# Performance work log

Measured on AMD Instinct MI355X. Metric: run time of the kernel, lower is better.

## Reference

```python
import jax, jax.numpy as jnp
import numpy as np

TEMP = 0.2
EPS = 1e-12  # F.normalize eps


def setup_inputs() -> dict:
    key = jax.random.key(0)
    k1, k2 = jax.random.split(key)
    l, B, K, D = 4, 64, 32, 128
    emb_i = jax.random.normal(k1, (l, B, K, D), dtype=jnp.float32)
    emb_j = jax.random.normal(k2, (l, B, K, D), dtype=jnp.float32)
    joint_valid = jnp.ones((B, K), dtype=jnp.float32)
    return {"emb_i": emb_i, "emb_j": emb_j, "joint_valid": joint_valid}


def _l2norm(x):
    n = jnp.sqrt(jnp.sum(x * x, axis=-1, keepdims=True))
    return x / jnp.maximum(n, EPS)


def reference(emb_i, emb_j, joint_valid):
    l, B, K, D = emb_i.shape
    N = B * K
    z_i = _l2norm(emb_i.reshape(l, N, D))
    z_j = _l2norm(emb_j.reshape(l, N, D))
    reps = jnp.concatenate([z_i, z_j], axis=1)              # (l, 2N, D), unit rows
    # cosine similarity of unit vectors == matmul
    sim = jnp.einsum('lnd,lmd->lnm', reps, reps)            # (l, 2N, 2N)
    idx = jnp.arange(N)
    pos = sim[:, idx, idx + N]                              # diag offset +N, (l, N)
    # note: original code uses the SAME +N offset diagonal for both ij and ji
    positives = jnp.concatenate([pos, pos], axis=1)         # (l, 2N)
    neg_mask = 1.0 - jnp.eye(2 * N, dtype=sim.dtype)        # (2N, 2N)
    denom = jnp.sum(neg_mask[None] * jnp.exp(sim / TEMP), axis=2)  # (l, 2N)
    loss_partial = -jnp.log(jnp.exp(positives / TEMP) / denom)    # (l, 2N)
    joints_mask = joint_valid.reshape(1, 1, B, K)
    all_num = jnp.sum(joint_valid)
    loss = jnp.sum(loss_partial.reshape(l, 2, B, K) * joints_mask) / (2.0 * all_num)
    return loss
```

## Files before the change

### kernel.cpp

```cpp
#include <hip/hip_runtime.h>
#include <hip/hip_bf16.h>

typedef __attribute__((ext_vector_type(8))) short short8;
typedef __attribute__((ext_vector_type(4))) float floatx4;

#define NROWS 4096
#define NHALF 2048
#define DDIM  128
#define LDST  136
#define SQRT_SCALE 2.6857914f
#define LN2 0.69314718056f

#define WS_ROWSUM_OFF 64
#define WS_DIAG_OFF   16448
#define WS_POS_OFF    32832
#define WS_Z_BYTE_OFF 196864

__device__ inline unsigned short f2bf(float f) {
    unsigned u = __builtin_bit_cast(unsigned, f);
    u += 0x7fffu + ((u >> 16) & 1u);
    return (unsigned short)(u >> 16);
}

__global__ __launch_bounds__(256) void k_norm(const float* __restrict__ emb_i,
                                              const float* __restrict__ emb_j,
                                              const float* __restrict__ jv,
                                              float* __restrict__ wsf,
                                              unsigned short* __restrict__ z) {
    int bx = blockIdx.x, tid = threadIdx.x;
    if (bx == 4096) {
        __shared__ float sred[256];
        float s = 0.f;
        #pragma unroll
        for (int i = 0; i < 8; ++i) s += jv[tid + 256 * i];
        sred[tid] = s; __syncthreads();
        for (int off = 128; off > 0; off >>= 1) {
            if (tid < off) sred[tid] += sred[tid + off];
            __syncthreads();
        }
        if (tid == 0) wsf[1] = sred[0];
        return;
    }
    int gid = bx * 256 + tid;
    if (gid == 0) { wsf[0] = 0.f; *(unsigned*)&wsf[2] = 0u; }
    if (gid >= WS_ROWSUM_OFF && gid < WS_ROWSUM_OFF + 16384) wsf[gid] = 0.f;

    int wave = tid >> 6, lane = tid & 63;
    int r = bx * 4 + wave;
    int l = r >> 12, n = r & 4095;
    const float* src = (n < NHALF) ? (emb_i + ((size_t)l * NHALF + n) * DDIM)
                                   : (emb_j + ((size_t)l * NHALF + (n - NHALF)) * DDIM);
    float2 v = *(const float2*)(src + lane * 2);
    float ss = v.x * v.x + v.y * v.y;
    #pragma unroll
    for (int off = 1; off < 64; off <<= 1) ss += __shfl_xor(ss, off);
    float inv = SQRT_SCALE / fmaxf(sqrtf(ss), 1e-12f);
    unsigned pack = ((unsigned)f2bf(v.y * inv) << 16) | (unsigned)f2bf(v.x * inv);
    *(unsigned*)(z + (size_t)r * DDIM + lane * 2) = pack;
}

__global__ __launch_bounds__(256, 4) void k_sim(const unsigned short* __restrict__ z,
                                                float* __restrict__ rowsum,
                                                float* __restrict__ diag,
                                                float* __restrict__ pos) {
    __shared__ __align__(16) unsigned short lds[128 * LDST];
    int bx = blockIdx.x, tid = threadIdx.x;
    int l = bx & 3, idx = bx >> 2;
    int J = (int)((sqrtf(8.f * (float)idx + 1.f) - 1.f) * 0.5f);
    while ((J + 1) * (J + 2) / 2 <= idx) ++J;
    while (J * (J + 1) / 2 > idx) --J;
    int I = idx - J * (J + 1) / 2;
    int wave = tid >> 6, lane = tid & 63, m = lane & 15, quad = lane >> 4;
    const unsigned short* zl = z + (size_t)l * NROWS * DDIM;
    int l4 = l * NROWS;
    int wr0 = I * 128 + wave * 32;
    int cg0 = J * 128;

    short8 a[2][4];
    #pragma unroll
    for (int rs = 0; rs < 2; ++rs) {
        const unsigned short* p = zl + (size_t)(wr0 + rs * 16 + m) * DDIM + quad * 8;
        #pragma unroll
        for (int kk = 0; kk < 4; ++kk) a[rs][kk] = *(const short8*)(p + kk * 32);
    }
    floatx4 rsum[2];
    #pragma unroll
    for (int rs = 0; rs < 2; ++rs) rsum[rs] = (floatx4){0.f, 0.f, 0.f, 0.f};
    float csum[8];
    #pragma unroll
    for (int g = 0; g < 8; ++g) csum[g] = 0.f;

    #pragma unroll
    for (int i = 0; i < 8; ++i) {
        int chunk = tid + 256 * i;
        int col = chunk >> 4, off = chunk & 15;
        uint4 d = *(const uint4*)(zl + (size_t)(cg0 + col) * DDIM + off * 8);
        *(uint4*)&lds[col * LDST + off * 8] = d;
    }
    __syncthreads();

    #pragma unroll
    for (int cs = 0; cs < 8; ++cs) {
        int ct = cg0 + cs * 16;
        const unsigned short* lp = &lds[(cs * 16 + m) * LDST + quad * 8];
        short8 b0 = *(const short8*)(lp);
        short8 b1 = *(const short8*)(lp + 32);
        short8 b2 = *(const short8*)(lp + 64);
        short8 b3 = *(const short8*)(lp + 96);
        #pragma unroll
        for (int rs = 0; rs < 2; ++rs) {
            floatx4 acc = (floatx4){0.f, 0.f, 0.f, 0.f};
            acc = __builtin_amdgcn_mfma_f32_16x16x32_bf16(a[rs][0], b0, acc, 0, 0, 0);
            acc = __builtin_amdgcn_mfma_f32_16x16x32_bf16(a[rs][1], b1, acc, 0, 0, 0);
            acc = __builtin_amdgcn_mfma_f32_16x16x32_bf16(a[rs][2], b2, acc, 0, 0, 0);
            acc = __builtin_amdgcn_mfma_f32_16x16x32_bf16(a[rs][3], b3, acc, 0, 0, 0);
            int rowbase = wr0 + rs * 16;
            bool isdiag = (ct == rowbase);
            bool ispos  = (ct == rowbase + 2048);
            if (isdiag || ispos) {
                int c = m - (quad << 2);
                if (c >= 0 && c < 4) {
                    float v = acc[c];
                    if (isdiag) diag[l4 + rowbase + m] = v;
                    else {
                        pos[l4 + rowbase + m] = v;
                        pos[l4 + rowbase + m + NHALF] = v;
                    }
                }
            }
            float t = 0.f;
            #pragma unroll
            for (int c = 0; c < 4; ++c) {
                float e = __builtin_amdgcn_exp2f(acc[c]);
                rsum[rs][c] += e;
                t += e;
            }
            csum[cs] += t;
        }
    }
    #pragma unroll
    for (int off = 1; off < 16; off <<= 1)
        #pragma unroll
        for (int rs = 0; rs < 2; ++rs)
            #pragma unroll
            for (int c = 0; c < 4; ++c)
                rsum[rs][c] += __shfl_xor(rsum[rs][c], off);
    if (m == 0) {
        #pragma unroll
        for (int rs = 0; rs < 2; ++rs)
            #pragma unroll
            for (int c = 0; c < 4; ++c) {
                int rg = wr0 + rs * 16 + quad * 4 + c;
                atomicAdd(&rowsum[l4 + rg], rsum[rs][c]);
            }
    }
    if (I != J) {
        __syncthreads();
        float* cred = (float*)lds;
        #pragma unroll
        for (int g = 0; g < 8; ++g) {
            float v = csum[g];
            v += __shfl_xor(v, 16);
            v += __shfl_xor(v, 32);
            if (quad == 0) cred[wave * 128 + g * 16 + m] = v;
        }
        __syncthreads();
        if (tid < 128) {
            float s = cred[tid] + cred[tid + 128] + cred[tid + 256] + cred[tid + 384];
            atomicAdd(&rowsum[l4 + cg0 + tid], s);
        }
    }
}

__global__ __launch_bounds__(256) void k_loss(const float* __restrict__ jv,
                                              const float* __restrict__ rowsum,
                                              const float* __restrict__ diag,
                                              const float* __restrict__ pos,
                                              float* __restrict__ wsf,
                                              float* __restrict__ out) {
    __shared__ float sred[256];
    int tid = threadIdx.x;
    int r = blockIdx.x * 256 + tid;
    int n = r & 4095;
    float denom = rowsum[r] - __builtin_amdgcn_exp2f(diag[r]);
    float contrib = LN2 * (__builtin_amdgcn_logf(denom) - pos[r]);
    float local = contrib * jv[n & (NHALF - 1)];
    sred[tid] = local; __syncthreads();
    for (int off = 128; off > 0; off >>= 1) {
        if (tid < off) sred[tid] += sred[tid + off];
        __syncthreads();
    }
    if (tid == 0) {
        atomicAdd(&wsf[0], sred[0]);
        __threadfence();
        unsigned c = atomicAdd((unsigned*)&wsf[2], 1u);
        if (c == 63) {
            float tot = atomicAdd(&wsf[0], 0.f);
            out[0] = tot / (2.f * wsf[1]);
        }
    }
}

extern "C" void kernel_launch(void* const* d_in, const int* in_sizes, int n_in,
                              void* d_out, int out_size, void* d_ws, size_t ws_size,
                              hipStream_t stream) {
    const float* emb_i = (const float*)d_in[0];
    const float* emb_j = (const float*)d_in[1];
    const float* jv    = (const float*)d_in[2];
    float* wsf    = (float*)d_ws;
    float* rowsum = wsf + WS_ROWSUM_OFF;
    float* diag   = wsf + WS_DIAG_OFF;
    float* pos    = wsf + WS_POS_OFF;
    unsigned short* z = (unsigned short*)((char*)d_ws + WS_Z_BYTE_OFF);
    float* out = (float*)d_out;

    k_norm <<<4097, 256, 0, stream>>>(emb_i, emb_j, jv, wsf, z);
    k_sim  <<<2112, 256, 0, stream>>>(z, rowsum, diag, pos);
    k_loss <<<64,   256, 0, stream>>>(jv, rowsum, diag, pos, wsf, out);
}
```

Measured before the change: 88.04 us.

## Pair row tiles per block and replace atomics with per-tile partial sums

Each k_sim block now handles two row tiles against one shared LDS column tile, which halves the grid and reuses each B-tile load across twice the MFMA work. Row and column exp-sums are written without atomics into a per-(layer, column tile) partial buffer. k_loss then sums 32 partials per row, so the zeroing pass in k_norm is removed. The costs are higher register pressure (launch bounds lowered to 3 blocks per CU), a larger workspace, and extra reads in k_loss.

After: 99.44 us. 12.9% more time.

```diff
diff --git a/kernel.cpp b/kernel.cpp
--- a/kernel.cpp
+++ b/kernel.cpp
@@ -11,10 +11,10 @@
 #define SQRT_SCALE 2.6857914f
 #define LN2 0.69314718056f
 
-#define WS_ROWSUM_OFF 64
-#define WS_DIAG_OFF   16448
-#define WS_POS_OFF    32832
-#define WS_Z_BYTE_OFF 196864
+#define WS_PART_OFF 64
+#define WS_DIAG_OFF 524352
+#define WS_POS_OFF  540736
+#define WS_Z_BYTE_OFF 2228480
 
 __device__ inline unsigned short f2bf(float f) {
     unsigned u = __builtin_bit_cast(unsigned, f);
@@ -41,9 +41,7 @@
         if (tid == 0) wsf[1] = sred[0];
         return;
     }
-    int gid = bx * 256 + tid;
-    if (gid == 0) { wsf[0] = 0.f; *(unsigned*)&wsf[2] = 0u; }
-    if (gid >= WS_ROWSUM_OFF && gid < WS_ROWSUM_OFF + 16384) wsf[gid] = 0.f;
+    if (bx == 0 && tid == 0) { wsf[0] = 0.f; *(unsigned*)&wsf[2] = 0u; }
 
     int wave = tid >> 6, lane = tid & 63;
     int r = bx * 4 + wave;
@@ -59,37 +57,38 @@
     *(unsigned*)(z + (size_t)r * DDIM + lane * 2) = pack;
 }
 
-__global__ __launch_bounds__(256, 4) void k_sim(const unsigned short* __restrict__ z,
-                                                float* __restrict__ rowsum,
+#define CPAIR(j) (((j) & 1) ? ((((j)+1)>>1)*(((j)+1)>>1)) : (((j)*((j)+2))>>2))
+__global__ __launch_bounds__(256, 3) void k_sim(const unsigned short* __restrict__ z,
+                                                float* __restrict__ part,
                                                 float* __restrict__ diag,
                                                 float* __restrict__ pos) {
     __shared__ __align__(16) unsigned short lds[128 * LDST];
+    __shared__ float cred[2][4][128];
     int bx = blockIdx.x, tid = threadIdx.x;
-    int l = bx & 3, idx = bx >> 2;
-    int J = (int)((sqrtf(8.f * (float)idx + 1.f) - 1.f) * 0.5f);
-    while ((J + 1) * (J + 2) / 2 <= idx) ++J;
-    while (J * (J + 1) / 2 > idx) --J;
-    int I = idx - J * (J + 1) / 2;
+    int l = bx & 3, q = bx >> 2;
+    int J = (int)(2.f * sqrtf((float)q + 0.25f));
+    if (J > 31) J = 31;
+    while (J < 31 && CPAIR(J + 1) <= q) ++J;
+    while (CPAIR(J) > q) --J;
+    int p = q - CPAIR(J);
+    int I0 = 2 * p;
+    bool two = (2 * p + 1 <= J);
+    int I1 = two ? (2 * p + 1) : I0;
+
     int wave = tid >> 6, lane = tid & 63, m = lane & 15, quad = lane >> 4;
     const unsigned short* zl = z + (size_t)l * NROWS * DDIM;
     int l4 = l * NROWS;
-    int wr0 = I * 128 + wave * 32;
     int cg0 = J * 128;
-
-    short8 a[2][4];
+    int wr00 = I0 * 128 + wave * 32;
+    int wr10 = I1 * 128 + wave * 32;
+
+    short8 a0[2][4], a1[2][4];
     #pragma unroll
     for (int rs = 0; rs < 2; ++rs) {
-        const unsigned short* p = zl + (size_t)(wr0 + rs * 16 + m) * DDIM + quad * 8;
-        #pragma unroll
-        for (int kk = 0; kk < 4; ++kk) a[rs][kk] = *(const short8*)(p + kk * 32);
-    }
-    floatx4 rsum[2];
-    #pragma unroll
-    for (int rs = 0; rs < 2; ++rs) rsum[rs] = (floatx4){0.f, 0.f, 0.f, 0.f};
-    float csum[8];
-    #pragma unroll
-    for (int g = 0; g < 8; ++g) csum[g] = 0.f;
-
+        const unsigned short* pa = zl + (size_t)(wr00 + rs * 16 + m) * DDIM + quad * 8;
+        #pragma unroll
+        for (int kk = 0; kk < 4; ++kk) a0[rs][kk] = *(const short8*)(pa + kk * 32);
+    }
     #pragma unroll
     for (int i = 0; i < 8; ++i) {
         int chunk = tid + 256 * i;
@@ -97,6 +96,21 @@
         uint4 d = *(const uint4*)(zl + (size_t)(cg0 + col) * DDIM + off * 8);
         *(uint4*)&lds[col * LDST + off * 8] = d;
     }
+    #pragma unroll
+    for (int rs = 0; rs < 2; ++rs) {
+        const unsigned short* pa = zl + (size_t)(wr10 + rs * 16 + m) * DDIM + quad * 8;
+        #pragma unroll
+        for (int kk = 0; kk < 4; ++kk) a1[rs][kk] = *(const short8*)(pa + kk * 32);
+    }
+    floatx4 rsum0[2], rsum1[2];
+    float csum0[8], csum1[8];
+    #pragma unroll
+    for (int rs = 0; rs < 2; ++rs) {
+        rsum0[rs] = (floatx4){0.f, 0.f, 0.f, 0.f};
+        rsum1[rs] = (floatx4){0.f, 0.f, 0.f, 0.f};
+    }
+    #pragma unroll
+    for (int g = 0; g < 8; ++g) { csum0[g] = 0.f; csum1[g] = 0.f; }
     __syncthreads();
 
     #pragma unroll
@@ -107,73 +121,91 @@
         short8 b1 = *(const short8*)(lp + 32);
         short8 b2 = *(const short8*)(lp + 64);
         short8 b3 = *(const short8*)(lp + 96);
+        float t0 = 0.f, t1 = 0.f;
         #pragma unroll
         for (int rs = 0; rs < 2; ++rs) {
-            floatx4 acc = (floatx4){0.f, 0.f, 0.f, 0.f};
-            acc = __builtin_amdgcn_mfma_f32_16x16x32_bf16(a[rs][0], b0, acc, 0, 0, 0);
-            acc = __builtin_amdgcn_mfma_f32_16x16x32_bf16(a[rs][1], b1, acc, 0, 0, 0);
-            acc = __builtin_amdgcn_mfma_f32_16x16x32_bf16(a[rs][2], b2, acc, 0, 0, 0);
-            acc = __builtin_amdgcn_mfma_f32_16x16x32_bf16(a[rs][3], b3, acc, 0, 0, 0);
-            int rowbase = wr0 + rs * 16;
-            bool isdiag = (ct == rowbase);
-            bool ispos  = (ct == rowbase + 2048);
-            if (isdiag || ispos) {
+            floatx4 p0 = (floatx4){0.f, 0.f, 0.f, 0.f};
+            floatx4 p1 = (floatx4){0.f, 0.f, 0.f, 0.f};
+            p0 = __builtin_amdgcn_mfma_f32_16x16x32_bf16(a0[rs][0], b0, p0, 0, 0, 0);
+            p1 = __builtin_amdgcn_mfma_f32_16x16x32_bf16(a1[rs][0], b0, p1, 0, 0, 0);
+            p0 = __builtin_amdgcn_mfma_f32_16x16x32_bf16(a0[rs][1], b1, p0, 0, 0, 0);
+            p1 = __builtin_amdgcn_mfma_f32_16x16x32_bf16(a1[rs][1], b1, p1, 0, 0, 0);
+            p0 = __builtin_amdgcn_mfma_f32_16x16x32_bf16(a0[rs][2], b2, p0, 0, 0, 0);
+            p1 = __builtin_amdgcn_mfma_f32_16x16x32_bf16(a1[rs][2], b2, p1, 0, 0, 0);
+            p0 = __builtin_amdgcn_mfma_f32_16x16x32_bf16(a0[rs][3], b3, p0, 0, 0, 0);
+            p1 = __builtin_amdgcn_mfma_f32_16x16x32_bf16(a1[rs][3], b3, p1, 0, 0, 0);
+            int rb0 = wr00 + rs * 16, rb1 = wr10 + rs * 16;
+            bool d0 = (ct == rb0), s0 = (ct == rb0 + 2048);
+            bool d1 = (ct == rb1), s1 = (ct == rb1 + 2048);
+            if (d0 || s0) {
                 int c = m - (quad << 2);
                 if (c >= 0 && c < 4) {
-                    float v = acc[c];
-                    if (isdiag) diag[l4 + rowbase + m] = v;
-                    else {
-                        pos[l4 + rowbase + m] = v;
-                        pos[l4 + rowbase + m + NHALF] = v;
-                    }
+                    float v = p0[c];
+                    if (d0) diag[l4 + rb0 + m] = v;
+                    else { pos[l4 + rb0 + m] = v; pos[l4 + rb0 + m + NHALF] = v; }
                 }
             }
-            float t = 0.f;
+            if (d1 || s1) {
+                int c = m - (quad << 2);
+                if (c >= 0 && c < 4) {
+                    float v = p1[c];
+                    if (d1) diag[l4 + rb1 + m] = v;
+                    else { pos[l4 + rb1 + m] = v; pos[l4 + rb1 + m + NHALF] = v; }
+                }
+            }
             #pragma unroll
             for (int c = 0; c < 4; ++c) {
-                float e = __builtin_amdgcn_exp2f(acc[c]);
-                rsum[rs][c] += e;
-                t += e;
-            }
-            csum[cs] += t;
-        }
+                float e0 = __builtin_amdgcn_exp2f(p0[c]);
+                float e1 = __builtin_amdgcn_exp2f(p1[c]);
+                rsum0[rs][c] += e0; t0 += e0;
+                rsum1[rs][c] += e1; t1 += e1;
+            }
+        }
+        csum0[cs] += t0;
+        csum1[cs] += t1;
     }
     #pragma unroll
     for (int off = 1; off < 16; off <<= 1)
-        #pragma unroll
-        for (int rs = 0; rs < 2; ++rs)
-            #pragma unroll
-            for (int c = 0; c < 4; ++c)
-                rsum[rs][c] += __shfl_xor(rsum[rs][c], off);
-    if (m == 0) {
         #pragma unroll
         for (int rs = 0; rs < 2; ++rs)
             #pragma unroll
             for (int c = 0; c < 4; ++c) {
-                int rg = wr0 + rs * 16 + quad * 4 + c;
-                atomicAdd(&rowsum[l4 + rg], rsum[rs][c]);
-            }
-    }
-    if (I != J) {
-        __syncthreads();
-        float* cred = (float*)lds;
-        #pragma unroll
-        for (int g = 0; g < 8; ++g) {
-            float v = csum[g];
-            v += __shfl_xor(v, 16);
-            v += __shfl_xor(v, 32);
-            if (quad == 0) cred[wave * 128 + g * 16 + m] = v;
-        }
-        __syncthreads();
-        if (tid < 128) {
-            float s = cred[tid] + cred[tid + 128] + cred[tid + 256] + cred[tid + 384];
-            atomicAdd(&rowsum[l4 + cg0 + tid], s);
+                rsum0[rs][c] += __shfl_xor(rsum0[rs][c], off);
+                rsum1[rs][c] += __shfl_xor(rsum1[rs][c], off);
+            }
+    float* plJ = part + (size_t)(l * 32 + J) * 4096;
+    if (m == 0) {
+        #pragma unroll
+        for (int rs = 0; rs < 2; ++rs)
+            #pragma unroll
+            for (int c = 0; c < 4; ++c) {
+                plJ[wr00 + rs * 16 + quad * 4 + c] = rsum0[rs][c];
+                if (two) plJ[wr10 + rs * 16 + quad * 4 + c] = rsum1[rs][c];
+            }
+    }
+    #pragma unroll
+    for (int g = 0; g < 8; ++g) {
+        float v0 = csum0[g]; v0 += __shfl_xor(v0, 16); v0 += __shfl_xor(v0, 32);
+        float v1 = csum1[g]; v1 += __shfl_xor(v1, 16); v1 += __shfl_xor(v1, 32);
+        if (quad == 0) { cred[0][wave][g * 16 + m] = v0; cred[1][wave][g * 16 + m] = v1; }
+    }
+    __syncthreads();
+    if (tid < 128) {
+        if (I0 != J) {
+            float s = cred[0][0][tid] + cred[0][1][tid] + cred[0][2][tid] + cred[0][3][tid];
+            part[(size_t)(l * 32 + I0) * 4096 + cg0 + tid] = s;
+        }
+    } else {
+        if (two && I1 != J) {
+            int t = tid - 128;
+            float s = cred[1][0][t] + cred[1][1][t] + cred[1][2][t] + cred[1][3][t];
+            part[(size_t)(l * 32 + I1) * 4096 + cg0 + t] = s;
         }
     }
 }
 
 __global__ __launch_bounds__(256) void k_loss(const float* __restrict__ jv,
-                                              const float* __restrict__ rowsum,
+                                              const float* __restrict__ part,
                                               const float* __restrict__ diag,
                                               const float* __restrict__ pos,
                                               float* __restrict__ wsf,
@@ -181,8 +213,12 @@
     __shared__ float sred[256];
     int tid = threadIdx.x;
     int r = blockIdx.x * 256 + tid;
-    int n = r & 4095;
-    float denom = rowsum[r] - __builtin_amdgcn_exp2f(diag[r]);
+    int l = r >> 12, n = r & 4095;
+    const float* pl = part + (size_t)l * 32 * 4096 + n;
+    float s = 0.f;
+    #pragma unroll
+    for (int k = 0; k < 32; ++k) s += pl[(size_t)k * 4096];
+    float denom = s - __builtin_amdgcn_exp2f(diag[r]);
     float contrib = LN2 * (__builtin_amdgcn_logf(denom) - pos[r]);
     float local = contrib * jv[n & (NHALF - 1)];
     sred[tid] = local; __syncthreads();
@@ -207,14 +243,14 @@
     const float* emb_i = (const float*)d_in[0];
     const float* emb_j = (const float*)d_in[1];
     const float* jv    = (const float*)d_in[2];
-    float* wsf    = (float*)d_ws;
-    float* rowsum = wsf + WS_ROWSUM_OFF;
-    float* diag   = wsf + WS_DIAG_OFF;
-    float* pos    = wsf + WS_POS_OFF;
+    float* wsf  = (float*)d_ws;
+    float* part = wsf + WS_PART_OFF;
+    float* diag = wsf + WS_DIAG_OFF;
+    float* pos  = wsf + WS_POS_OFF;
     unsigned short* z = (unsigned short*)((char*)d_ws + WS_Z_BYTE_OFF);
     float* out = (float*)d_out;
 
     k_norm <<<4097, 256, 0, stream>>>(emb_i, emb_j, jv, wsf, z);
-    k_sim  <<<2112, 256, 0, stream>>>(z, rowsum, diag, pos);
-    k_loss <<<64,   256, 0, stream>>>(jv, rowsum, diag, pos, wsf, out);
-}
+    k_sim  <<<1088, 256, 0, stream>>>(z, part, diag, pos);
+    k_loss <<<64,   256, 0, stream>>>(jv, part, diag, pos, wsf, out);
+}
```
